# Kernel tuning notes

Measured on AMD Instinct MI355X. Metric: run time of the kernel, lower is better.

The kernel has to match this reference:

```python
import jax, jax.numpy as jnp
import numpy as np

NUM_GROUPS1 = 8
NUM_GROUPS2 = 4
NUM_HEADS = 8


def setup_inputs() -> dict:
    key = jax.random.key(0)
    k1, k2, k3 = jax.random.split(key, 3)
    B, N, C = 8, 4096, 512
    x = jax.random.normal(k1, (B, N, C), dtype=jnp.float32)
    # torch Linear(dim, 3*inner_dim, bias=False); stored transposed for x @ W
    W_qkv = jax.random.normal(k2, (C, 3 * C), dtype=jnp.float32) * 0.02
    W_proj = jax.random.normal(k3, (C, C), dtype=jnp.float32) * 0.02
    b_proj = jnp.zeros((C,), dtype=jnp.float32)
    return {"x": x, "W_qkv": W_qkv, "W_proj": W_proj, "b_proj": b_proj,
            "recursive_index": 0}


def reference(x, W_qkv, W_proj, b_proj, recursive_index):
    # recursive_index is a static Python int (0 -> False branch, num_groups1).
    num_groups = NUM_GROUPS1 if not recursive_index else NUM_GROUPS2
    B, N, C = x.shape
    H = NUM_HEADS
    Dh = C // H
    scale = Dh ** -0.5
    Np = int(np.ceil(N / num_groups) * num_groups)
    if Np != N:
        x = jnp.pad(x, ((0, 0), (0, Np - N), (0, 0)))
    L = Np // num_groups  # tokens per group
    # qkv projection, then split into per-group per-head tensors [B,G,H,L,Dh]
    qkv = (x @ W_qkv).reshape(B, num_groups, L, 3, H, Dh)
    q = jnp.transpose(qkv[:, :, :, 0], (0, 1, 3, 2, 4))
    k = jnp.transpose(qkv[:, :, :, 1], (0, 1, 3, 2, 4))
    v = jnp.transpose(qkv[:, :, :, 2], (0, 1, 3, 2, 4))
    attn = jax.nn.softmax(jnp.einsum('bghld,bghmd->bghlm', q, k) * scale, axis=-1)
    out = jnp.einsum('bghlm,bghmd->bghld', attn, v)  # [B,G,H,L,Dh]
    out = jnp.transpose(out, (0, 1, 3, 2, 4)).reshape(B, Np, C)[:, :N]
    return out @ W_proj + b_proj
```

## Files before the change

### kernel.cpp

```cpp
#include <hip/hip_runtime.h>
#include <hip/hip_bf16.h>

typedef __attribute__((ext_vector_type(8))) short  bf16x8;
typedef __attribute__((ext_vector_type(4))) float  f32x4;

__device__ __forceinline__ ushort f2bf(float f) {
    unsigned u = __builtin_bit_cast(unsigned, f);
    u += 0x7fffu + ((u >> 16) & 1u);
    return (ushort)(u >> 16);
}

__device__ __forceinline__ unsigned cvt_pk_bf16(float a, float b) {
    unsigned r;
    asm("v_cvt_pk_bf16_f32 %0, %1, %2" : "=v"(r) : "v"(a), "v"(b));
    return r;
}

__device__ __forceinline__ void gload_lds16(const ushort* g, ushort* l) {
    __builtin_amdgcn_global_load_lds(
        (const __attribute__((address_space(1))) void*)(g),
        (__attribute__((address_space(3))) void*)(l), 16, 0, 0);
}

__global__ __launch_bounds__(256) void prep_kernel(
        const float* __restrict__ x, ushort* __restrict__ xb,
        const float* __restrict__ Wqkv, ushort* __restrict__ wq,
        const float* __restrict__ Wproj, ushort* __restrict__ wp) {
    __shared__ ushort t[64 * 65];
    const int bx = blockIdx.x, tid = threadIdx.x;
    if (bx < 16384) {
        int i = bx * 256 + tid;
        float4 f = reinterpret_cast<const float4*>(x)[i];
        ushort4 o;
        o.x = f2bf(f.x); o.y = f2bf(f.y); o.z = f2bf(f.z); o.w = f2bf(f.w);
        reinterpret_cast<ushort4*>(xb)[i] = o;
        return;
    }
    const float* in; ushort* out; int Cc, qcols, cB, rB; float qs;
    if (bx < 16576) {
        int b2 = bx - 16384;
        in = Wqkv; out = wq; Cc = 1536; qcols = 512;
        qs = 0.18033688011112043f;
        cB = (b2 % 24) * 64; rB = (b2 / 24) * 64;
    } else {
        int b2 = bx - 16576;
        in = Wproj; out = wp; Cc = 512; qcols = 0; qs = 1.0f;
        cB = (b2 % 8) * 64; rB = (b2 / 8) * 64;
    }
#pragma unroll
    for (int p = 0; p < 16; ++p) {
        int lin = p * 256 + tid;
        int r = lin >> 6, c = lin & 63;
        float v = in[(size_t)(rB + r) * Cc + cB + c];
        if (cB + c < qcols) v *= qs;
        t[c * 65 + r] = f2bf(v);
    }
    __syncthreads();
#pragma unroll
    for (int p = 0; p < 16; ++p) {
        int lin = p * 256 + tid;
        int c = lin >> 6, r = lin & 63;
        out[(size_t)(cB + c) * 512 + rB + r] = t[c * 65 + r];
    }
}

template<bool F32OUT, bool SPLIT_VT>
__global__ __launch_bounds__(256) void gemm_bt_kernel(
        const ushort* __restrict__ A, const ushort* __restrict__ Bt,
        void* __restrict__ Cout, const float* __restrict__ bias,
        const ushort* __restrict__ Wv, ushort* __restrict__ vT,
        int Ncols, int K) {
    __shared__ ushort smem[16384];
    const int tid  = threadIdx.x;
    const int id = blockIdx.x;
    const bool vt = SPLIT_VT && (id >= 2048);
    const ushort* Amat; const ushort* Bmat; int mBase, nBase;
    if (!vt) {
        Amat = A; Bmat = Bt;
        mBase = ((id & 7) * 32 + ((id >> 3) & 31)) << 7;
        nBase = (id >> 8) << 7;
    } else {
        int vid = id - 2048;
        Amat = Wv; Bmat = A;
        mBase = (vid >> 8) << 7;
        nBase = ((vid & 7) * 32 + ((vid >> 3) & 31)) << 7;
    }
    const int w = tid >> 6, lane = tid & 63, ml = lane & 15, quad = lane >> 4;
    const int wr = (w >> 1) << 6, wc = (w & 1) << 6;

    const int srow = lane >> 2;
    const int sch  = (lane & 3) ^ ((lane >> 3) & 3);
    const ushort* Ap = Amat + (size_t)(mBase + w * 32 + srow) * K + sch * 8;
    const ushort* Bp = Bmat + (size_t)(nBase + w * 32 + srow) * K + sch * 8;

    f32x4 z4 = {0.f, 0.f, 0.f, 0.f};
    f32x4 acc[4][4];
#pragma unroll
    for (int i = 0; i < 4; ++i)
#pragma unroll
        for (int j = 0; j < 4; ++j) acc[i][j] = z4;

    auto stagef = [&](int kt, int buf) {
        ushort* la_ = smem + buf * 8192;
        ushort* lb_ = la_ + 4096;
        const ushort* a = Ap + kt * 32;
        const ushort* b = Bp + kt * 32;
        gload_lds16(a,            la_ + (w * 32) * 32);
        gload_lds16(a + 16 * K,   la_ + (w * 32 + 16) * 32);
        gload_lds16(b,            lb_ + (w * 32) * 32);
        gload_lds16(b + 16 * K,   lb_ + (w * 32 + 16) * 32);
    };

    const int nkt = K >> 5;
    const int rdoff = (quad ^ ((ml >> 1) & 3)) << 3;
    stagef(0, 0);
    __syncthreads();
    int cur = 0;
    for (int kt = 0; kt < nkt; ++kt) {
        if (kt + 1 < nkt) stagef(kt + 1, cur ^ 1);
        ushort* la_ = smem + cur * 8192;
        ushort* lb_ = la_ + 4096;
        bf16x8 af[4], bv[4];
#pragma unroll
        for (int i = 0; i < 4; ++i)
            af[i] = *reinterpret_cast<bf16x8*>(la_ + (wr + i * 16 + ml) * 32 + rdoff);
#pragma unroll
        for (int j = 0; j < 4; ++j)
            bv[j] = *reinterpret_cast<bf16x8*>(lb_ + (wc + j * 16 + ml) * 32 + rdoff);
#pragma unroll
        for (int i = 0; i < 4; ++i)
#pragma unroll
            for (int j = 0; j < 4; ++j)
                acc[i][j] = __builtin_amdgcn_mfma_f32_16x16x32_bf16(af[i], bv[j], acc[i][j], 0, 0, 0);
        __syncthreads();
        cur ^= 1;
    }

    if (F32OUT) {
        float* ep = reinterpret_cast<float*>(smem) + w * 1088;
        float bj[4];
#pragma unroll
        for (int j = 0; j < 4; ++j) bj[j] = bias[nBase + wc + j * 16 + ml];
        float* cbase = reinterpret_cast<float*>(Cout);
#pragma unroll
        for (int i = 0; i < 4; ++i) {
#pragma unroll
            for (int j = 0; j < 4; ++j)
#pragma unroll
                for (int r = 0; r < 4; ++r)
                    ep[(quad * 4 + r) * 68 + j * 16 + ml] = acc[i][j][r] + bj[j];
#pragma unroll
            for (int t = 0; t < 4; ++t) {
                int ch = quad + 4 * t;
                float4 v = *reinterpret_cast<const float4*>(ep + ml * 68 + ch * 4);
                *reinterpret_cast<float4*>(cbase
                    + (size_t)(mBase + wr + i * 16 + ml) * Ncols + nBase + wc + ch * 4) = v;
            }
        }
    } else {
        ushort* ep = smem + w * 1152;
#pragma unroll
        for (int i = 0; i < 4; ++i) {
#pragma unroll
            for (int j = 0; j < 4; ++j)
#pragma unroll
                for (int r = 0; r < 4; ++r)
                    ep[(quad * 4 + r) * 72 + j * 16 + ml] = f2bf(acc[i][j][r]);
#pragma unroll
            for (int t = 0; t < 2; ++t) {
                int ch = quad + 4 * t;
                bf16x8 v = *reinterpret_cast<const bf16x8*>(ep + ml * 72 + ch * 8);
                int row = mBase + wr + i * 16 + ml;
                if (!vt) {
                    *reinterpret_cast<bf16x8*>(reinterpret_cast<ushort*>(Cout)
                        + (size_t)row * Ncols + nBase + wc + ch * 8) = v;
                } else {
                    *reinterpret_cast<bf16x8*>(vT
                        + ((size_t)((nBase >> 9) * 512 + row)) * 512
                        + (nBase & 511) + wc + ch * 8) = v;
                }
            }
        }
    }
}

__global__ __launch_bounds__(256) void attn_kernel(
        const ushort* __restrict__ qk, const ushort* __restrict__ vT,
        ushort* __restrict__ out) {
    __shared__ ushort k_lds[64 * 64];
    __shared__ ushort v_lds[64 * 64];
    __shared__ ushort p_lds[4 * 32 * 72];
    const int tid = threadIdx.x;
    const int w = tid >> 6, lane = tid & 63, ml = lane & 15, quad = lane >> 4;
    const int id = blockIdx.x;
    const int bgh = id >> 2, qc = id & 3;
    const int b = bgh >> 6, g = (bgh >> 3) & 7, h = bgh & 7;
    const int tb = b * 4096 + g * 512;
    const ushort* base  = qk + (size_t)tb * 1024 + h * 64;
    const ushort* vbase = vT + ((size_t)((b * 8 + g) * 512 + h * 64)) * 512;
    const int qOff = qc * 128 + w * 32;

    bf16x8 qf[2][2];
#pragma unroll
    for (int qb = 0; qb < 2; ++qb)
#pragma unroll
        for (int ks = 0; ks < 2; ++ks)
            qf[qb][ks] = *reinterpret_cast<const bf16x8*>(
                base + (size_t)(qOff + qb * 16 + ml) * 1024 + ks * 32 + quad * 8);

    const int srow = lane >> 3;
    const int sch  = (lane & 7) ^ srow;
    const ushort* kp = base + (size_t)(w * 16 + srow) * 1024 + 512 + sch * 8;
    ushort* kdst = k_lds + (w * 16) * 64;
    const ushort* vp = vbase + (size_t)(w * 16 + srow) * 512 + sch * 8;
    ushort* vdst = v_lds + (w * 16) * 64;

    const bf16x8 onesf = {0x3f80, 0x3f80, 0x3f80, 0x3f80,
                          0x3f80, 0x3f80, 0x3f80, 0x3f80};

    f32x4 z4 = {0.f, 0.f, 0.f, 0.f};
    f32x4 oacc[2][4];
    f32x4 sacc[2];
#pragma unroll
    for (int qb = 0; qb < 2; ++qb) {
#pragma unroll
        for (int db = 0; db < 4; ++db) oacc[qb][db] = z4;
        sacc[qb] = z4;
    }

    ushort* pw = p_lds + w * 32 * 72;
    for (int kt = 0; kt < 8; ++kt) {
        gload_lds16(kp + (size_t)(kt * 64) * 1024,     kdst);
        gload_lds16(kp + (size_t)(kt * 64 + 8) * 1024, kdst + 8 * 64);
        gload_lds16(vp + kt * 64,           vdst);
        gload_lds16(vp + 8 * 512 + kt * 64, vdst + 8 * 64);
        __syncthreads();

        f32x4 s[2][4];
#pragma unroll
        for (int qb = 0; qb < 2; ++qb)
#pragma unroll
            for (int kb = 0; kb < 4; ++kb) s[qb][kb] = z4;
#pragma unroll
        for (int ks = 0; ks < 2; ++ks) {
            bf16x8 kfs[4];
#pragma unroll
            for (int kb = 0; kb < 4; ++kb)
                kfs[kb] = *reinterpret_cast<bf16x8*>(
                    k_lds + (kb * 16 + ml) * 64 + (((ks * 4 + quad) ^ (ml & 7)) << 3));
#pragma unroll
            for (int qb = 0; qb < 2; ++qb)
#pragma unroll
                for (int kb = 0; kb < 4; ++kb)
                    s[qb][kb] = __builtin_amdgcn_mfma_f32_16x16x32_bf16(kfs[kb], qf[qb][ks], s[qb][kb], 0, 0, 0);
        }

#pragma unroll
        for (int qb = 0; qb < 2; ++qb)
#pragma unroll
            for (int kb = 0; kb < 4; ++kb) {
                float p0 = exp2f(s[qb][kb][0]), p1 = exp2f(s[qb][kb][1]);
                float p2 = exp2f(s[qb][kb][2]), p3 = exp2f(s[qb][kb][3]);
                uint2 pk2;
                pk2.x = cvt_pk_bf16(p0, p1);
                pk2.y = cvt_pk_bf16(p2, p3);
                *reinterpret_cast<uint2*>(
                    pw + (qb * 16 + ml) * 72 + kb * 16 + quad * 4) = pk2;
            }

#pragma unroll
        for (int ks = 0; ks < 2; ++ks) {
            bf16x8 pfs[2], vfs[4];
#pragma unroll
            for (int qb = 0; qb < 2; ++qb)
                pfs[qb] = *reinterpret_cast<bf16x8*>(
                    pw + (qb * 16 + ml) * 72 + ks * 32 + quad * 8);
#pragma unroll
            for (int db = 0; db < 4; ++db)
                vfs[db] = *reinterpret_cast<bf16x8*>(
                    v_lds + (db * 16 + ml) * 64 + (((ks * 4 + quad) ^ (ml & 7)) << 3));
#pragma unroll
            for (int qb = 0; qb < 2; ++qb)
                sacc[qb] = __builtin_amdgcn_mfma_f32_16x16x32_bf16(pfs[qb], onesf, sacc[qb], 0, 0, 0);
#pragma unroll
            for (int qb = 0; qb < 2; ++qb)
#pragma unroll
                for (int db = 0; db < 4; ++db)
                    oacc[qb][db] = __builtin_amdgcn_mfma_f32_16x16x32_bf16(pfs[qb], vfs[db], oacc[qb][db], 0, 0, 0);
        }
        __syncthreads();
    }

    float invq[2][4];
#pragma unroll
    for (int qb = 0; qb < 2; ++qb)
#pragma unroll
        for (int r = 0; r < 4; ++r)
            invq[qb][r] = 1.0f / sacc[qb][r];
#pragma unroll
    for (int qb = 0; qb < 2; ++qb)
#pragma unroll
        for (int db = 0; db < 4; ++db)
#pragma unroll
            for (int r = 0; r < 4; ++r) {
                float v = oacc[qb][db][r] * invq[qb][r];
                out[(size_t)(tb + qOff + qb * 16 + quad * 4 + r) * 512
                    + h * 64 + db * 16 + ml] = f2bf(v);
            }
}

extern "C" void kernel_launch(void* const* d_in, const int* in_sizes, int n_in,
                              void* d_out, int out_size, void* d_ws, size_t ws_size,
                              hipStream_t stream) {
    const float* x     = (const float*)d_in[0];
    const float* Wqkv  = (const float*)d_in[1];
    const float* Wproj = (const float*)d_in[2];
    const float* bproj = (const float*)d_in[3];

    char* ws = (char*)d_ws;
    ushort* xb   = (ushort*)(ws);
    ushort* wq   = (ushort*)(ws + 33554432);
    ushort* wp   = (ushort*)(ws + 35127296);
    ushort* qkb  = (ushort*)(ws + 35651584);
    ushort* vTb  = (ushort*)(ws + 102760448);
    ushort* attn = xb;
    ushort* wv   = wq + 1024 * 512;
    float*  outp = (float*)d_out;

    prep_kernel<<<16640, 256, 0, stream>>>(x, xb, Wqkv, wq, Wproj, wp);
    gemm_bt_kernel<false, true><<<3072, 256, 0, stream>>>(
        xb, wq, qkb, nullptr, wv, vTb, 1024, 512);
    attn_kernel<<<2048, 256, 0, stream>>>(qkb, vTb, attn);
    gemm_bt_kernel<true, false><<<1024, 256, 0, stream>>>(
        attn, wp, outp, bproj, nullptr, nullptr, 512, 512);
}
```

Baseline: 299.6 us.

## Enlarge GEMM tiles to 256x256 with 8 waves and deeper K pipeline

```diff
diff --git a/kernel.cpp b/kernel.cpp
--- a/kernel.cpp
+++ b/kernel.cpp
@@ -21,6 +21,15 @@
         (const __attribute__((address_space(1))) void*)(g),
         (__attribute__((address_space(3))) void*)(l), 16, 0, 0);
 }
+
+__device__ __forceinline__ void blockbar() {
+    asm volatile("" ::: "memory");
+    __builtin_amdgcn_sched_barrier(0);
+    __builtin_amdgcn_s_barrier();
+    __builtin_amdgcn_sched_barrier(0);
+    asm volatile("" ::: "memory");
+}
+#define SFENCE() __builtin_amdgcn_sched_barrier(0)
 
 __global__ __launch_bounds__(256) void prep_kernel(
         const float* __restrict__ x, ushort* __restrict__ xb,
@@ -65,76 +74,101 @@
 }
 
 template<bool F32OUT, bool SPLIT_VT>
-__global__ __launch_bounds__(256) void gemm_bt_kernel(
+__global__ __launch_bounds__(512, 2) void gemm_bt_kernel(
         const ushort* __restrict__ A, const ushort* __restrict__ Bt,
         void* __restrict__ Cout, const float* __restrict__ bias,
         const ushort* __restrict__ Wv, ushort* __restrict__ vT,
         int Ncols, int K) {
-    __shared__ ushort smem[16384];
-    const int tid  = threadIdx.x;
-    const int id = blockIdx.x;
-    const bool vt = SPLIT_VT && (id >= 2048);
+    __shared__ ushort smem[65536];
+    const int tid = threadIdx.x;
+    const int id  = blockIdx.x;
+    const bool vt = SPLIT_VT && (id >= 512);
     const ushort* Amat; const ushort* Bmat; int mBase, nBase;
     if (!vt) {
         Amat = A; Bmat = Bt;
-        mBase = ((id & 7) * 32 + ((id >> 3) & 31)) << 7;
-        nBase = (id >> 8) << 7;
+        mBase = ((id & 7) * 16 + ((id >> 3) & 15)) << 8;
+        nBase = (id >> 7) << 8;
     } else {
-        int vid = id - 2048;
+        int vid = id - 512;
         Amat = Wv; Bmat = A;
-        mBase = (vid >> 8) << 7;
-        nBase = ((vid & 7) * 32 + ((vid >> 3) & 31)) << 7;
+        mBase = (vid >> 7) << 8;
+        nBase = ((vid & 7) * 16 + ((vid >> 3) & 15)) << 8;
     }
     const int w = tid >> 6, lane = tid & 63, ml = lane & 15, quad = lane >> 4;
-    const int wr = (w >> 1) << 6, wc = (w & 1) << 6;
-
-    const int srow = lane >> 2;
-    const int sch  = (lane & 3) ^ ((lane >> 3) & 3);
+    const int wr = (w >> 2) * 128, wc = (w & 3) * 64;
+
+    const int srow = lane >> 3;
+    const int sch  = (lane & 7) ^ srow;
     const ushort* Ap = Amat + (size_t)(mBase + w * 32 + srow) * K + sch * 8;
     const ushort* Bp = Bmat + (size_t)(nBase + w * 32 + srow) * K + sch * 8;
 
     f32x4 z4 = {0.f, 0.f, 0.f, 0.f};
-    f32x4 acc[4][4];
-#pragma unroll
-    for (int i = 0; i < 4; ++i)
+    f32x4 acc[8][4];
+#pragma unroll
+    for (int i = 0; i < 8; ++i)
 #pragma unroll
         for (int j = 0; j < 4; ++j) acc[i][j] = z4;
 
-    auto stagef = [&](int kt, int buf) {
-        ushort* la_ = smem + buf * 8192;
-        ushort* lb_ = la_ + 4096;
-        const ushort* a = Ap + kt * 32;
-        const ushort* b = Bp + kt * 32;
-        gload_lds16(a,            la_ + (w * 32) * 32);
-        gload_lds16(a + 16 * K,   la_ + (w * 32 + 16) * 32);
-        gload_lds16(b,            lb_ + (w * 32) * 32);
-        gload_lds16(b + 16 * K,   lb_ + (w * 32 + 16) * 32);
+    auto stage = [&](int t, int slot) {
+        ushort* la_ = smem + slot * 32768;
+        ushort* lb_ = la_ + 16384;
+        const ushort* a = Ap + t * 64;
+        const ushort* b = Bp + t * 64;
+#pragma unroll
+        for (int i = 0; i < 4; ++i) {
+            gload_lds16(a + (size_t)(8 * i) * K, la_ + (w * 32 + 8 * i) * 64);
+            gload_lds16(b + (size_t)(8 * i) * K, lb_ + (w * 32 + 8 * i) * 64);
+        }
     };
 
-    const int nkt = K >> 5;
-    const int rdoff = (quad ^ ((ml >> 1) & 3)) << 3;
-    stagef(0, 0);
-    __syncthreads();
-    int cur = 0;
-    for (int kt = 0; kt < nkt; ++kt) {
-        if (kt + 1 < nkt) stagef(kt + 1, cur ^ 1);
-        ushort* la_ = smem + cur * 8192;
-        ushort* lb_ = la_ + 4096;
-        bf16x8 af[4], bv[4];
-#pragma unroll
-        for (int i = 0; i < 4; ++i)
-            af[i] = *reinterpret_cast<bf16x8*>(la_ + (wr + i * 16 + ml) * 32 + rdoff);
-#pragma unroll
-        for (int j = 0; j < 4; ++j)
-            bv[j] = *reinterpret_cast<bf16x8*>(lb_ + (wc + j * 16 + ml) * 32 + rdoff);
-#pragma unroll
-        for (int i = 0; i < 4; ++i)
-#pragma unroll
-            for (int j = 0; j < 4; ++j)
-                acc[i][j] = __builtin_amdgcn_mfma_f32_16x16x32_bf16(af[i], bv[j], acc[i][j], 0, 0, 0);
-        __syncthreads();
-        cur ^= 1;
-    }
+    const int rdo0 = ((0 + quad) ^ (ml & 7)) << 3;
+    const int rdo1 = ((4 + quad) ^ (ml & 7)) << 3;
+
+    auto compute = [&](int slot) {
+        ushort* la_ = smem + slot * 32768;
+        ushort* lb_ = la_ + 16384;
+        bf16x8 bv[4][2];
+#pragma unroll
+        for (int fn = 0; fn < 4; ++fn) {
+            ushort* r = lb_ + (wc + fn * 16 + ml) * 64;
+            bv[fn][0] = *reinterpret_cast<bf16x8*>(r + rdo0);
+            bv[fn][1] = *reinterpret_cast<bf16x8*>(r + rdo1);
+        }
+#pragma unroll
+        for (int mh = 0; mh < 2; ++mh) {
+            bf16x8 af[4][2];
+#pragma unroll
+            for (int fm = 0; fm < 4; ++fm) {
+                ushort* r = la_ + (wr + mh * 64 + fm * 16 + ml) * 64;
+                af[fm][0] = *reinterpret_cast<bf16x8*>(r + rdo0);
+                af[fm][1] = *reinterpret_cast<bf16x8*>(r + rdo1);
+            }
+            __builtin_amdgcn_s_setprio(1);
+#pragma unroll
+            for (int ks = 0; ks < 2; ++ks)
+#pragma unroll
+                for (int fm = 0; fm < 4; ++fm)
+#pragma unroll
+                    for (int fn = 0; fn < 4; ++fn)
+                        acc[mh * 4 + fm][fn] = __builtin_amdgcn_mfma_f32_16x16x32_bf16(
+                            af[fm][ks], bv[fn][ks], acc[mh * 4 + fm][fn], 0, 0, 0);
+            __builtin_amdgcn_s_setprio(0);
+        }
+    };
+
+    const int nkt = K >> 6;
+    stage(0, 0); SFENCE();
+    stage(1, 1); SFENCE();
+    for (int t = 0; t < nkt - 1; ++t) {
+        asm volatile("s_waitcnt vmcnt(8)" ::: "memory");
+        blockbar();
+        compute(t & 1);
+        blockbar();
+        if (t + 2 < nkt) { stage(t + 2, t & 1); SFENCE(); }
+    }
+    asm volatile("s_waitcnt vmcnt(0)" ::: "memory");
+    blockbar();
+    compute((nkt - 1) & 1);
 
     if (F32OUT) {
         float* ep = reinterpret_cast<float*>(smem) + w * 1088;
@@ -143,7 +177,7 @@
         for (int j = 0; j < 4; ++j) bj[j] = bias[nBase + wc + j * 16 + ml];
         float* cbase = reinterpret_cast<float*>(Cout);
 #pragma unroll
-        for (int i = 0; i < 4; ++i) {
+        for (int i = 0; i < 8; ++i) {
 #pragma unroll
             for (int j = 0; j < 4; ++j)
 #pragma unroll
@@ -160,7 +194,7 @@
     } else {
         ushort* ep = smem + w * 1152;
 #pragma unroll
-        for (int i = 0; i < 4; ++i) {
+        for (int i = 0; i < 8; ++i) {
 #pragma unroll
             for (int j = 0; j < 4; ++j)
 #pragma unroll
@@ -328,9 +362,9 @@
     float*  outp = (float*)d_out;
 
     prep_kernel<<<16640, 256, 0, stream>>>(x, xb, Wqkv, wq, Wproj, wp);
-    gemm_bt_kernel<false, true><<<3072, 256, 0, stream>>>(
+    gemm_bt_kernel<false, true><<<768, 512, 0, stream>>>(
         xb, wq, qkb, nullptr, wv, vTb, 1024, 512);
     attn_kernel<<<2048, 256, 0, stream>>>(qkb, vTb, attn);
-    gemm_bt_kernel<true, false><<<1024, 256, 0, stream>>>(
+    gemm_bt_kernel<true, false><<<256, 512, 0, stream>>>(
         attn, wp, outp, bproj, nullptr, nullptr, 512, 512);
 }
```

After: 279.9 us. 1.07x faster.

## Restructure GEMM K-loop with explicit vmcnt waits, raise MFMA priority, remap attention blocks

Applied to the files above, without the earlier changes.

```diff
diff --git a/kernel.cpp b/kernel.cpp
--- a/kernel.cpp
+++ b/kernel.cpp
@@ -21,6 +21,15 @@
         (const __attribute__((address_space(1))) void*)(g),
         (__attribute__((address_space(3))) void*)(l), 16, 0, 0);
 }
+
+__device__ __forceinline__ void blockbar() {
+    asm volatile("" ::: "memory");
+    __builtin_amdgcn_sched_barrier(0);
+    __builtin_amdgcn_s_barrier();
+    __builtin_amdgcn_sched_barrier(0);
+    asm volatile("" ::: "memory");
+}
+#define SFENCE() __builtin_amdgcn_sched_barrier(0)
 
 __global__ __launch_bounds__(256) void prep_kernel(
         const float* __restrict__ x, ushort* __restrict__ xb,
@@ -71,8 +80,8 @@
         const ushort* __restrict__ Wv, ushort* __restrict__ vT,
         int Ncols, int K) {
     __shared__ ushort smem[16384];
-    const int tid  = threadIdx.x;
-    const int id = blockIdx.x;
+    const int tid = threadIdx.x;
+    const int id  = blockIdx.x;
     const bool vt = SPLIT_VT && (id >= 2048);
     const ushort* Amat; const ushort* Bmat; int mBase, nBase;
     if (!vt) {
@@ -100,25 +109,21 @@
 #pragma unroll
         for (int j = 0; j < 4; ++j) acc[i][j] = z4;
 
-    auto stagef = [&](int kt, int buf) {
-        ushort* la_ = smem + buf * 8192;
+    auto stage = [&](int t, int slot) {
+        ushort* la_ = smem + slot * 8192;
         ushort* lb_ = la_ + 4096;
-        const ushort* a = Ap + kt * 32;
-        const ushort* b = Bp + kt * 32;
-        gload_lds16(a,            la_ + (w * 32) * 32);
-        gload_lds16(a + 16 * K,   la_ + (w * 32 + 16) * 32);
-        gload_lds16(b,            lb_ + (w * 32) * 32);
-        gload_lds16(b + 16 * K,   lb_ + (w * 32 + 16) * 32);
+        const ushort* a = Ap + t * 32;
+        const ushort* b = Bp + t * 32;
+        gload_lds16(a,          la_ + (w * 32) * 32);
+        gload_lds16(a + 16 * K, la_ + (w * 32 + 16) * 32);
+        gload_lds16(b,          lb_ + (w * 32) * 32);
+        gload_lds16(b + 16 * K, lb_ + (w * 32 + 16) * 32);
     };
 
-    const int nkt = K >> 5;
     const int rdoff = (quad ^ ((ml >> 1) & 3)) << 3;
-    stagef(0, 0);
-    __syncthreads();
-    int cur = 0;
-    for (int kt = 0; kt < nkt; ++kt) {
-        if (kt + 1 < nkt) stagef(kt + 1, cur ^ 1);
-        ushort* la_ = smem + cur * 8192;
+
+    auto compute = [&](int slot) {
+        ushort* la_ = smem + slot * 8192;
         ushort* lb_ = la_ + 4096;
         bf16x8 af[4], bv[4];
 #pragma unroll
@@ -127,16 +132,31 @@
 #pragma unroll
         for (int j = 0; j < 4; ++j)
             bv[j] = *reinterpret_cast<bf16x8*>(lb_ + (wc + j * 16 + ml) * 32 + rdoff);
+        __builtin_amdgcn_s_setprio(1);
 #pragma unroll
         for (int i = 0; i < 4; ++i)
 #pragma unroll
             for (int j = 0; j < 4; ++j)
                 acc[i][j] = __builtin_amdgcn_mfma_f32_16x16x32_bf16(af[i], bv[j], acc[i][j], 0, 0, 0);
-        __syncthreads();
-        cur ^= 1;
-    }
+        __builtin_amdgcn_s_setprio(0);
+    };
+
+    const int nkt = K >> 5;
+    stage(0, 0); SFENCE();
+    stage(1, 1); SFENCE();
+    for (int t = 0; t < nkt - 1; ++t) {
+        asm volatile("s_waitcnt vmcnt(4)" ::: "memory");
+        blockbar();
+        compute(t & 1);
+        blockbar();
+        if (t + 2 < nkt) { stage(t + 2, t & 1); SFENCE(); }
+    }
+    asm volatile("s_waitcnt vmcnt(0)" ::: "memory");
+    blockbar();
+    compute((nkt - 1) & 1);
 
     if (F32OUT) {
+        blockbar();
         float* ep = reinterpret_cast<float*>(smem) + w * 1088;
         float bj[4];
 #pragma unroll
@@ -193,7 +213,8 @@
     const int tid = threadIdx.x;
     const int w = tid >> 6, lane = tid & 63, ml = lane & 15, quad = lane >> 4;
     const int id = blockIdx.x;
-    const int bgh = id >> 2, qc = id & 3;
+    const int qc = (id >> 3) & 3;
+    const int bgh = (id & 7) | ((id >> 5) << 3);
     const int b = bgh >> 6, g = (bgh >> 3) & 7, h = bgh & 7;
     const int tb = b * 4096 + g * 512;
     const ushort* base  = qk + (size_t)tb * 1024 + h * 64;
@@ -248,11 +269,13 @@
             for (int kb = 0; kb < 4; ++kb)
                 kfs[kb] = *reinterpret_cast<bf16x8*>(
                     k_lds + (kb * 16 + ml) * 64 + (((ks * 4 + quad) ^ (ml & 7)) << 3));
+            __builtin_amdgcn_s_setprio(1);
 #pragma unroll
             for (int qb = 0; qb < 2; ++qb)
 #pragma unroll
                 for (int kb = 0; kb < 4; ++kb)
                     s[qb][kb] = __builtin_amdgcn_mfma_f32_16x16x32_bf16(kfs[kb], qf[qb][ks], s[qb][kb], 0, 0, 0);
+            __builtin_amdgcn_s_setprio(0);
         }
 
 #pragma unroll
@@ -279,6 +302,7 @@
             for (int db = 0; db < 4; ++db)
                 vfs[db] = *reinterpret_cast<bf16x8*>(
                     v_lds + (db * 16 + ml) * 64 + (((ks * 4 + quad) ^ (ml & 7)) << 3));
+            __builtin_amdgcn_s_setprio(1);
 #pragma unroll
             for (int qb = 0; qb < 2; ++qb)
                 sacc[qb] = __builtin_amdgcn_mfma_f32_16x16x32_bf16(pfs[qb], onesf, sacc[qb], 0, 0, 0);
@@ -287,6 +311,7 @@
 #pragma unroll
                 for (int db = 0; db < 4; ++db)
                     oacc[qb][db] = __builtin_amdgcn_mfma_f32_16x16x32_bf16(pfs[qb], vfs[db], oacc[qb][db], 0, 0, 0);
+            __builtin_amdgcn_s_setprio(0);
         }
         __syncthreads();
     }
```

Result: no change. 298.3 us (-0.4%).
